# Performance work log

Hardware: AMD Instinct MI355X
Metric: run time of the kernel (lower is better)

The kernel has to match this reference:

```python
import jax, jax.numpy as jnp
import numpy as np
from jax import lax

RATIO = 2.0
ITERATIONS = 1


def setup_inputs() -> dict:
    key = jax.random.key(0)
    k1, k2 = jax.random.split(key)
    N, H, W = 64, 512, 512
    x = jax.random.normal(k1, (N, H, W), dtype=jnp.float32)  # logits
    y = jax.random.randint(k2, (N, H, W), 0, 2, dtype=jnp.int32)  # binary labels
    return {"x": x, "y": y}


def _erode(m):
    # cv2.erode with 3x3 all-ones kernel == 3x3 min-pool; cv2 default border
    # value for erode is +inf, matching reduce_window's init_value padding.
    return lax.reduce_window(m, jnp.inf, lax.min, (1, 3, 3), (1, 1, 1), 'SAME')


def _dilate(m):
    # cv2.dilate == 3x3 max-pool; default border value -inf == init_value pad.
    return lax.reduce_window(m, -jnp.inf, lax.max, (1, 3, 3), (1, 1, 1), 'SAME')


def reference(x, y):
    yf = y.astype(x.dtype)
    # elementwise BCE-with-logits (reduction='none'), numerically stable
    loss = jnp.maximum(x, 0.0) - x * yf + jnp.log1p(jnp.exp(-jnp.abs(x)))
    m = (y > 0).astype(x.dtype)  # [N,H,W] binary mask
    ero, dil = m, m
    for _ in range(ITERATIONS):
        ero = _erode(ero)
        dil = _dilate(dil)
    border = dil - ero  # 1 on border pixels, 0 elsewhere
    w = border * RATIO + (1.0 - border)
    return (loss * w).mean()
```

## Files before the change

### kernel.cpp

```cpp
#include <hip/hip_runtime.h>
#include <math.h>

#define NIMG 64
#define HH 512
#define WW 512
#define TR 8
#define ROWSTRIDE 520
#define LROWS (TR + 2)
#define NBLOCKS (NIMG * (HH / TR))
#define INV_TOTAL (1.0f / 16777216.0f)

__global__ __launch_bounds__(256) void border_loss_main(
    const float* __restrict__ x, const int* __restrict__ y,
    float* __restrict__ part, int atomic_mode)
{
    __shared__ unsigned char flags[LROWS * ROWSTRIDE];
    __shared__ float wsum[4];

    const int tid = threadIdx.x;
    const int nb  = blockIdx.x;
    const int n   = nb >> 6;
    const int R0  = (nb & 63) * TR;
    const long long imgbase = (long long)n * HH * WW;

    if (tid < LROWS) {
        unsigned char* row = &flags[tid * ROWSTRIDE];
        row[0] = 0; row[513] = 0; row[514] = 0; row[515] = 0;
    }

    #pragma unroll
    for (int it = 0; it < 5; ++it) {
        int idx = tid + it * 256;
        int j = idx >> 7;
        int g = idx & 127;
        int gr = R0 - 1 + j;
        unsigned int f4 = 0;
        if ((unsigned)gr < (unsigned)HH) {
            const int4 yv = *(const int4*)(y + imgbase + (long long)gr * WW + 4 * g);
            f4  = (yv.x > 0 ? 1u : 2u);
            f4 |= (yv.y > 0 ? 1u : 2u) << 8;
            f4 |= (yv.z > 0 ? 1u : 2u) << 16;
            f4 |= (yv.w > 0 ? 1u : 2u) << 24;
        }
        unsigned char* p = &flags[j * ROWSTRIDE + 4 * g + 1];
        p[0] = (unsigned char)(f4);
        p[1] = (unsigned char)(f4 >> 8);
        p[2] = (unsigned char)(f4 >> 16);
        p[3] = (unsigned char)(f4 >> 24);
    }
    __syncthreads();

    float acc = 0.0f;

    #pragma unroll
    for (int it = 0; it < 4; ++it) {
        int idx = tid + it * 256;
        int r = idx >> 7;
        int g = idx & 127;
        const unsigned int* l0 = (const unsigned int*)&flags[(r    ) * ROWSTRIDE + 4 * g];
        const unsigned int* l1 = (const unsigned int*)&flags[(r + 1) * ROWSTRIDE + 4 * g];
        const unsigned int* l2 = (const unsigned int*)&flags[(r + 2) * ROWSTRIDE + 4 * g];
        unsigned long long v0 = (unsigned long long)l0[0] | ((unsigned long long)l0[1] << 32);
        unsigned long long v1 = (unsigned long long)l1[0] | ((unsigned long long)l1[1] << 32);
        unsigned long long v2 = (unsigned long long)l2[0] | ((unsigned long long)l2[1] << 32);
        unsigned long long v = v0 | v1 | v2;
        unsigned long long h = v | (v >> 8) | (v >> 16);

        const float4 xv = *(const float4*)(x + imgbase + (long long)(R0 + r) * WW + 4 * g);
        const float xs[4] = {xv.x, xv.y, xv.z, xv.w};
        #pragma unroll
        for (int k = 0; k < 4; ++k) {
            float xf = xs[k];
            float m = (float)((unsigned)(v1 >> (8 * (k + 1))) & 1u);
            float l = fmaxf(xf, 0.0f) - xf * m + log1pf(expf(-fabsf(xf)));
            float wgt = (((unsigned)(h >> (8 * k)) & 3u) == 3u) ? 2.0f : 1.0f;
            acc += l * wgt;
        }
    }

    #pragma unroll
    for (int off = 32; off > 0; off >>= 1)
        acc += __shfl_down(acc, off);
    if ((tid & 63) == 0) wsum[tid >> 6] = acc;
    __syncthreads();
    if (tid == 0) {
        float s = wsum[0] + wsum[1] + wsum[2] + wsum[3];
        if (atomic_mode) atomicAdd(part, s * INV_TOTAL);
        else             part[blockIdx.x] = s;
    }
}

__global__ __launch_bounds__(256) void border_loss_reduce(
    const float* __restrict__ part, float* __restrict__ out)
{
    __shared__ float wsum[4];
    float s = 0.0f;
    for (int i = threadIdx.x; i < NBLOCKS; i += 256) s += part[i];
    #pragma unroll
    for (int off = 32; off > 0; off >>= 1)
        s += __shfl_down(s, off);
    if ((threadIdx.x & 63) == 0) wsum[threadIdx.x >> 6] = s;
    __syncthreads();
    if (threadIdx.x == 0)
        out[0] = (wsum[0] + wsum[1] + wsum[2] + wsum[3]) * INV_TOTAL;
}

__global__ void border_loss_zero(float* out) { out[0] = 0.0f; }

extern "C" void kernel_launch(void* const* d_in, const int* in_sizes, int n_in,
                              void* d_out, int out_size, void* d_ws, size_t ws_size,
                              hipStream_t stream)
{
    const float* x = (const float*)d_in[0];
    const int*   y = (const int*)d_in[1];
    float* out = (float*)d_out;

    if (ws_size >= (size_t)NBLOCKS * sizeof(float)) {
        float* part = (float*)d_ws;
        border_loss_main<<<NBLOCKS, 256, 0, stream>>>(x, y, part, 0);
        border_loss_reduce<<<1, 256, 0, stream>>>(part, out);
    } else {
        border_loss_zero<<<1, 1, 0, stream>>>(out);
        border_loss_main<<<NBLOCKS, 256, 0, stream>>>(x, y, out, 1);
    }
}
```

Before: 169.4 us.

## Encode label masks as wave-ballot bitmasks and compute borders with bit shifts

Replaces the byte-per-pixel shared flag array with 64-bit ballot bitmasks for the mask and its complement. Erosion and dilation become row ORs plus shifts with carries across segments. It also enlarges tiles to 32 rows with 512-thread blocks, which cuts halo rereads of y from 25% to about 6%, and switches to fast __expf/__logf intrinsics. Loads drop from 16-byte vectors to 4-byte per-lane coalesced loads, and the fast math intrinsics may slightly change accuracy.

```diff
diff --git a/kernel.cpp b/kernel.cpp
--- a/kernel.cpp
+++ b/kernel.cpp
@@ -4,87 +4,90 @@
 #define NIMG 64
 #define HH 512
 #define WW 512
-#define TR 8
-#define ROWSTRIDE 520
+#define TR 32
+#define NSEG 8
 #define LROWS (TR + 2)
 #define NBLOCKS (NIMG * (HH / TR))
 #define INV_TOTAL (1.0f / 16777216.0f)
 
-__global__ __launch_bounds__(256) void border_loss_main(
+__global__ __launch_bounds__(512) void border_loss_main(
     const float* __restrict__ x, const int* __restrict__ y,
     float* __restrict__ part, int atomic_mode)
 {
-    __shared__ unsigned char flags[LROWS * ROWSTRIDE];
-    __shared__ float wsum[4];
+    __shared__ unsigned long long mm[LROWS][NSEG];
+    __shared__ unsigned long long mz[LROWS][NSEG];
+    __shared__ float wsum[8];
 
-    const int tid = threadIdx.x;
-    const int nb  = blockIdx.x;
-    const int n   = nb >> 6;
-    const int R0  = (nb & 63) * TR;
+    const int tid  = threadIdx.x;
+    const int lane = tid & 63;
+    const int w    = tid >> 6;
+    const int nb   = blockIdx.x;
+    const int n    = nb >> 4;
+    const int R0   = (nb & 15) * TR;
     const long long imgbase = (long long)n * HH * WW;
 
-    if (tid < LROWS) {
-        unsigned char* row = &flags[tid * ROWSTRIDE];
-        row[0] = 0; row[513] = 0; row[514] = 0; row[515] = 0;
-    }
-
-    #pragma unroll
-    for (int it = 0; it < 5; ++it) {
-        int idx = tid + it * 256;
-        int j = idx >> 7;
-        int g = idx & 127;
+    for (int T = w; T < LROWS * NSEG; T += 8) {
+        int j = T >> 3;
+        int s = T & 7;
         int gr = R0 - 1 + j;
-        unsigned int f4 = 0;
+        unsigned long long bm = 0ull, bz = 0ull;
         if ((unsigned)gr < (unsigned)HH) {
-            const int4 yv = *(const int4*)(y + imgbase + (long long)gr * WW + 4 * g);
-            f4  = (yv.x > 0 ? 1u : 2u);
-            f4 |= (yv.y > 0 ? 1u : 2u) << 8;
-            f4 |= (yv.z > 0 ? 1u : 2u) << 16;
-            f4 |= (yv.w > 0 ? 1u : 2u) << 24;
+            int yv = y[imgbase + (long long)gr * WW + (s << 6) + lane];
+            bm = __ballot(yv > 0);
+            bz = ~bm;
         }
-        unsigned char* p = &flags[j * ROWSTRIDE + 4 * g + 1];
-        p[0] = (unsigned char)(f4);
-        p[1] = (unsigned char)(f4 >> 8);
-        p[2] = (unsigned char)(f4 >> 16);
-        p[3] = (unsigned char)(f4 >> 24);
+        if (lane == 0) { mm[j][s] = bm; mz[j][s] = bz; }
     }
     __syncthreads();
 
     float acc = 0.0f;
+    #pragma unroll
+    for (int k = 0; k < TR / 8; ++k) {
+        int rr = w + (k << 3);
+        int jr = rr + 1;
+        const float* xrow = x + imgbase + (long long)(R0 + rr) * WW;
 
-    #pragma unroll
-    for (int it = 0; it < 4; ++it) {
-        int idx = tid + it * 256;
-        int r = idx >> 7;
-        int g = idx & 127;
-        const unsigned int* l0 = (const unsigned int*)&flags[(r    ) * ROWSTRIDE + 4 * g];
-        const unsigned int* l1 = (const unsigned int*)&flags[(r + 1) * ROWSTRIDE + 4 * g];
-        const unsigned int* l2 = (const unsigned int*)&flags[(r + 2) * ROWSTRIDE + 4 * g];
-        unsigned long long v0 = (unsigned long long)l0[0] | ((unsigned long long)l0[1] << 32);
-        unsigned long long v1 = (unsigned long long)l1[0] | ((unsigned long long)l1[1] << 32);
-        unsigned long long v2 = (unsigned long long)l2[0] | ((unsigned long long)l2[1] << 32);
-        unsigned long long v = v0 | v1 | v2;
-        unsigned long long h = v | (v >> 8) | (v >> 16);
+        unsigned long long vm_prev = 0ull, vz_prev = 0ull;
+        unsigned long long vm_cur = mm[jr-1][0] | mm[jr][0] | mm[jr+1][0];
+        unsigned long long vz_cur = mz[jr-1][0] | mz[jr][0] | mz[jr+1][0];
 
-        const float4 xv = *(const float4*)(x + imgbase + (long long)(R0 + r) * WW + 4 * g);
-        const float xs[4] = {xv.x, xv.y, xv.z, xv.w};
         #pragma unroll
-        for (int k = 0; k < 4; ++k) {
-            float xf = xs[k];
-            float m = (float)((unsigned)(v1 >> (8 * (k + 1))) & 1u);
-            float l = fmaxf(xf, 0.0f) - xf * m + log1pf(expf(-fabsf(xf)));
-            float wgt = (((unsigned)(h >> (8 * k)) & 3u) == 3u) ? 2.0f : 1.0f;
-            acc += l * wgt;
+        for (int s = 0; s < NSEG; ++s) {
+            unsigned long long vm_next = 0ull, vz_next = 0ull;
+            if (s + 1 < NSEG) {
+                vm_next = mm[jr-1][s+1] | mm[jr][s+1] | mm[jr+1][s+1];
+                vz_next = mz[jr-1][s+1] | mz[jr][s+1] | mz[jr+1][s+1];
+            }
+            unsigned long long hm = vm_cur | (vm_cur << 1) | (vm_cur >> 1)
+                                  | (vm_prev >> 63) | (vm_next << 63);
+            unsigned long long hz = vz_cur | (vz_cur << 1) | (vz_cur >> 1)
+                                  | (vz_prev >> 63) | (vz_next << 63);
+            unsigned long long border = hm & hz;
+            unsigned long long mrow   = mm[jr][s];
+
+            float xf = xrow[(s << 6) + lane];
+            float a  = fabsf(xf);
+            float lg = __logf(1.0f + __expf(-a));
+            float mterm = ((mrow >> lane) & 1ull) ? xf : 0.0f;
+            float loss  = fmaxf(xf, 0.0f) - mterm + lg;
+            float wgt   = ((border >> lane) & 1ull) ? 2.0f : 1.0f;
+            acc = fmaf(loss, wgt, acc);
+
+            vm_prev = vm_cur; vz_prev = vz_cur;
+            vm_cur  = vm_next; vz_cur  = vz_next;
         }
     }
 
     #pragma unroll
     for (int off = 32; off > 0; off >>= 1)
         acc += __shfl_down(acc, off);
-    if ((tid & 63) == 0) wsum[tid >> 6] = acc;
+    __syncthreads();
+    if (lane == 0) wsum[w] = acc;
     __syncthreads();
     if (tid == 0) {
-        float s = wsum[0] + wsum[1] + wsum[2] + wsum[3];
+        float s = 0.0f;
+        #pragma unroll
+        for (int i = 0; i < 8; ++i) s += wsum[i];
         if (atomic_mode) atomicAdd(part, s * INV_TOTAL);
         else             part[blockIdx.x] = s;
     }
@@ -117,10 +120,10 @@
 
     if (ws_size >= (size_t)NBLOCKS * sizeof(float)) {
         float* part = (float*)d_ws;
-        border_loss_main<<<NBLOCKS, 256, 0, stream>>>(x, y, part, 0);
+        border_loss_main<<<NBLOCKS, 512, 0, stream>>>(x, y, part, 0);
         border_loss_reduce<<<1, 256, 0, stream>>>(part, out);
     } else {
         border_loss_zero<<<1, 1, 0, stream>>>(out);
-        border_loss_main<<<NBLOCKS, 256, 0, stream>>>(x, y, out, 1);
+        border_loss_main<<<NBLOCKS, 512, 0, stream>>>(x, y, out, 1);
     }
 }
```

After: 164.0 us. -3.2%, faster.

## Replace LDS halo tile with per-wave register row streaming and lane shuffles

Applied to the files above, without the earlier changes.

Each wave now owns a half-row strip of 8 rows and walks down them, keeping the three label rows' flags in registers and exchanging horizontal neighbours with lane shuffles and a scalar boundary load, instead of staging a 10-row halo in shared memory with a block barrier. The next row's x and y are prefetched while the current row is computed. Fast __expf/__logf intrinsics replace log1pf/expf. This removes LDS traffic and the sync, and cuts the halo re-read ratio per tile. In exchange it adds shuffle work and small precision differences from the fast intrinsics.

```diff
diff --git a/kernel.cpp b/kernel.cpp
--- a/kernel.cpp
+++ b/kernel.cpp
@@ -4,89 +4,116 @@
 #define NIMG 64
 #define HH 512
 #define WW 512
-#define TR 8
-#define ROWSTRIDE 520
-#define LROWS (TR + 2)
-#define NBLOCKS (NIMG * (HH / TR))
+#define SH 8
+#define NBLOCKS (NIMG * 32)
 #define INV_TOTAL (1.0f / 16777216.0f)
 
-__global__ __launch_bounds__(256) void border_loss_main(
+typedef unsigned int u32;
+
+__device__ __forceinline__ u32 flags4(int4 yv) {
+    u32 f = (yv.x > 0) ? 1u : 2u;
+    f |= ((yv.y > 0) ? 1u : 2u) << 8;
+    f |= ((yv.z > 0) ? 1u : 2u) << 16;
+    f |= ((yv.w > 0) ? 1u : 2u) << 24;
+    return f;
+}
+
+__global__ __launch_bounds__(256, 8) void border_loss_main(
     const float* __restrict__ x, const int* __restrict__ y,
     float* __restrict__ part, int atomic_mode)
 {
-    __shared__ unsigned char flags[LROWS * ROWSTRIDE];
     __shared__ float wsum[4];
 
-    const int tid = threadIdx.x;
-    const int nb  = blockIdx.x;
-    const int n   = nb >> 6;
-    const int R0  = (nb & 63) * TR;
-    const long long imgbase = (long long)n * HH * WW;
+    const int tid  = threadIdx.x;
+    const int lane = tid & 63;
+    const int w    = tid >> 6;
+    const int b    = blockIdx.x;
+    const int n    = b >> 5;
+    const int q    = ((b & 31) << 2) | w;
+    const int g    = q & 1;
+    const int R0   = (q >> 1) * SH;
+    const int base = n * (HH * WW);
+    const int colv = (g << 8) | (lane << 2);
+    const int cb   = 256 - g;
+    const int*   __restrict__ yb = y + base;
+    const float* __restrict__ xb = x + base;
+    const int idxL = (lane + 63) & 63;
+    const int idxR = (lane + 1) & 63;
 
-    if (tid < LROWS) {
-        unsigned char* row = &flags[tid * ROWSTRIDE];
-        row[0] = 0; row[513] = 0; row[514] = 0; row[515] = 0;
+#define YVEC(row) (*(const int4*)(yb + (row) * WW + colv))
+#define XVEC(row) (*(const float4*)(xb + (row) * WW + colv))
+#define YBND(row) (yb[__builtin_amdgcn_readfirstlane((row) * WW + cb)])
+
+    u32 f_t = 0u, bF_t = 0u;
+    if (R0 > 0) {
+        f_t  = flags4(YVEC(R0 - 1));
+        bF_t = (YBND(R0 - 1) > 0) ? 1u : 2u;
     }
+    u32 f_c  = flags4(YVEC(R0));
+    u32 bF_c = (YBND(R0) > 0) ? 1u : 2u;
+
+    const int pr0 = (R0 + 1 < HH) ? R0 + 1 : HH - 1;
+    int4   y4_b = YVEC(pr0);
+    int    bY_b = YBND(pr0);
+    float4 x4_c = XVEC(R0);
+
+    float acc0 = 0.0f, acc1 = 0.0f;
 
     #pragma unroll
-    for (int it = 0; it < 5; ++it) {
-        int idx = tid + it * 256;
-        int j = idx >> 7;
-        int g = idx & 127;
-        int gr = R0 - 1 + j;
-        unsigned int f4 = 0;
-        if ((unsigned)gr < (unsigned)HH) {
-            const int4 yv = *(const int4*)(y + imgbase + (long long)gr * WW + 4 * g);
-            f4  = (yv.x > 0 ? 1u : 2u);
-            f4 |= (yv.y > 0 ? 1u : 2u) << 8;
-            f4 |= (yv.z > 0 ? 1u : 2u) << 16;
-            f4 |= (yv.w > 0 ? 1u : 2u) << 24;
+    for (int r = 0; r < SH; ++r) {
+        const int gr = R0 + r;
+
+        int4 y4_n; int bY_n; float4 x4_n;
+        if (r < SH - 1) {
+            const int pry = (gr + 2 < HH) ? gr + 2 : HH - 1;
+            y4_n = YVEC(pry);
+            bY_n = YBND(pry);
+            x4_n = XVEC(gr + 1);
         }
-        unsigned char* p = &flags[j * ROWSTRIDE + 4 * g + 1];
-        p[0] = (unsigned char)(f4);
-        p[1] = (unsigned char)(f4 >> 8);
-        p[2] = (unsigned char)(f4 >> 16);
-        p[3] = (unsigned char)(f4 >> 24);
-    }
-    __syncthreads();
 
-    float acc = 0.0f;
+        const bool vB = (gr + 1 < HH);
+        const u32 f_b  = vB ? flags4(y4_b) : 0u;
+        const u32 bF_b = vB ? ((bY_b > 0) ? 1u : 2u) : 0u;
 
-    #pragma unroll
-    for (int it = 0; it < 4; ++it) {
-        int idx = tid + it * 256;
-        int r = idx >> 7;
-        int g = idx & 127;
-        const unsigned int* l0 = (const unsigned int*)&flags[(r    ) * ROWSTRIDE + 4 * g];
-        const unsigned int* l1 = (const unsigned int*)&flags[(r + 1) * ROWSTRIDE + 4 * g];
-        const unsigned int* l2 = (const unsigned int*)&flags[(r + 2) * ROWSTRIDE + 4 * g];
-        unsigned long long v0 = (unsigned long long)l0[0] | ((unsigned long long)l0[1] << 32);
-        unsigned long long v1 = (unsigned long long)l1[0] | ((unsigned long long)l1[1] << 32);
-        unsigned long long v2 = (unsigned long long)l2[0] | ((unsigned long long)l2[1] << 32);
-        unsigned long long v = v0 | v1 | v2;
-        unsigned long long h = v | (v >> 8) | (v >> 16);
+        const u32 v   = f_t | f_c | f_b;
+        const u32 bFv = bF_t | bF_c | bF_b;
+        const u32 vL  = __shfl(v, idxL);
+        const u32 vR  = __shfl(v, idxR);
+        const u32 inL = (lane == 0)  ? (g ? bFv : 0u) : (vL >> 24);
+        const u32 inR = (lane == 63) ? (g ? 0u : bFv) : (vR & 0xffu);
+        const u32 h   = v | (v << 8) | (v >> 8) | inL | (inR << 24);
+        const u32 bm  = h & (h >> 1) & 0x01010101u;
 
-        const float4 xv = *(const float4*)(x + imgbase + (long long)(R0 + r) * WW + 4 * g);
-        const float xs[4] = {xv.x, xv.y, xv.z, xv.w};
+        const float xs[4] = {x4_c.x, x4_c.y, x4_c.z, x4_c.w};
         #pragma unroll
         for (int k = 0; k < 4; ++k) {
-            float xf = xs[k];
-            float m = (float)((unsigned)(v1 >> (8 * (k + 1))) & 1u);
-            float l = fmaxf(xf, 0.0f) - xf * m + log1pf(expf(-fabsf(xf)));
-            float wgt = (((unsigned)(h >> (8 * k)) & 3u) == 3u) ? 2.0f : 1.0f;
-            acc += l * wgt;
+            const float xf = xs[k];
+            const float lg = __logf(1.0f + __expf(-fabsf(xf)));
+            const bool mbit = (f_c >> (8 * k)) & 1u;
+            const bool bbit = (bm  >> (8 * k)) & 1u;
+            const float loss = fmaxf(xf, 0.0f) - (mbit ? xf : 0.0f) + lg;
+            if (k & 1) acc1 = fmaf(loss, bbit ? 2.0f : 1.0f, acc1);
+            else       acc0 = fmaf(loss, bbit ? 2.0f : 1.0f, acc0);
         }
+
+        f_t = f_c;  f_c = f_b;
+        bF_t = bF_c; bF_c = bF_b;
+        if (r < SH - 1) { y4_b = y4_n; bY_b = bY_n; x4_c = x4_n; }
     }
+#undef YVEC
+#undef XVEC
+#undef YBND
 
+    float acc = acc0 + acc1;
     #pragma unroll
     for (int off = 32; off > 0; off >>= 1)
         acc += __shfl_down(acc, off);
-    if ((tid & 63) == 0) wsum[tid >> 6] = acc;
+    if (lane == 0) wsum[w] = acc;
     __syncthreads();
     if (tid == 0) {
-        float s = wsum[0] + wsum[1] + wsum[2] + wsum[3];
-        if (atomic_mode) atomicAdd(part, s * INV_TOTAL);
-        else             part[blockIdx.x] = s;
+        const float t = wsum[0] + wsum[1] + wsum[2] + wsum[3];
+        if (atomic_mode) atomicAdd(part, t * INV_TOTAL);
+        else             part[blockIdx.x] = t;
     }
 }
 
@@ -94,12 +121,12 @@
     const float* __restrict__ part, float* __restrict__ out)
 {
     __shared__ float wsum[4];
-    float s = 0.0f;
-    for (int i = threadIdx.x; i < NBLOCKS; i += 256) s += part[i];
+    float t = 0.0f;
+    for (int i = threadIdx.x; i < NBLOCKS; i += 256) t += part[i];
     #pragma unroll
     for (int off = 32; off > 0; off >>= 1)
-        s += __shfl_down(s, off);
-    if ((threadIdx.x & 63) == 0) wsum[threadIdx.x >> 6] = s;
+        t += __shfl_down(t, off);
+    if ((threadIdx.x & 63) == 0) wsum[threadIdx.x >> 6] = t;
     __syncthreads();
     if (threadIdx.x == 0)
         out[0] = (wsum[0] + wsum[1] + wsum[2] + wsum[3]) * INV_TOTAL;
```

Measured after the change: 188.6 us. 1.11x slower.

## Replace LDS halo tiling with direct global neighbor loads and fast math

Applied to the files above, without the earlier changes.

Removes the shared-memory flag tile and per-block sync; each thread now loads its own float4 of x plus the 3x6 neighbourhood of labels straight from global memory, relying on cache for the redundant row reads. Computes erosion/dilation via bitwise AND/OR on the raw labels. Swaps log1pf/expf for __logf/__expf intrinsics and launches one thread per four pixels with more blocks. Redundant label reads raise cache traffic, and fast intrinsics slightly reduce accuracy.

```diff
diff --git a/kernel.cpp b/kernel.cpp
--- a/kernel.cpp
+++ b/kernel.cpp
@@ -4,78 +4,91 @@
 #define NIMG 64
 #define HH 512
 #define WW 512
-#define TR 8
-#define ROWSTRIDE 520
-#define LROWS (TR + 2)
-#define NBLOCKS (NIMG * (HH / TR))
+#define NPIX (NIMG * HH * WW)
+#define NTHREADS (NPIX / 4)
+#define NBLK (NTHREADS / 256)
 #define INV_TOTAL (1.0f / 16777216.0f)
 
-__global__ __launch_bounds__(256) void border_loss_main(
+__global__ __launch_bounds__(256, 8) void border_loss_main(
     const float* __restrict__ x, const int* __restrict__ y,
     float* __restrict__ part, int atomic_mode)
 {
-    __shared__ unsigned char flags[LROWS * ROWSTRIDE];
     __shared__ float wsum[4];
 
     const int tid = threadIdx.x;
-    const int nb  = blockIdx.x;
-    const int n   = nb >> 6;
-    const int R0  = (nb & 63) * TR;
-    const long long imgbase = (long long)n * HH * WW;
+    const int idx = blockIdx.x * 256 + tid;
+    const int g   = idx & 127;
+    const int r   = (idx >> 7) & (HH - 1);
+    const int n   = idx >> 16;
+    const int rowb = n * (HH * WW) + r * WW;
+    const int c0  = g << 2;
 
-    if (tid < LROWS) {
-        unsigned char* row = &flags[tid * ROWSTRIDE];
-        row[0] = 0; row[513] = 0; row[514] = 0; row[515] = 0;
+    const int offT = (r > 0)      ? -WW : 0;
+    const int offB = (r < HH - 1) ?  WW : 0;
+    const int cL   = (g == 0)     ? 0        : (c0 - 1);
+    const int cR   = (g == 127)   ? (WW - 1) : (c0 + 4);
+
+    const int4 yC = *(const int4*)(y + rowb + c0);
+    const int4 yT = *(const int4*)(y + rowb + offT + c0);
+    const int4 yB = *(const int4*)(y + rowb + offB + c0);
+    const int yCL = y[rowb + cL];
+    const int yTL = y[rowb + offT + cL];
+    const int yBL = y[rowb + offB + cL];
+    const int yCR = y[rowb + cR];
+    const int yTR = y[rowb + offT + cR];
+    const int yBR = y[rowb + offB + cR];
+    const float4 xv = *(const float4*)(x + rowb + c0);
+
+    const int vo0 = yT.x | yC.x | yB.x;
+    const int vo1 = yT.y | yC.y | yB.y;
+    const int vo2 = yT.z | yC.z | yB.z;
+    const int vo3 = yT.w | yC.w | yB.w;
+    const int va0 = yT.x & yC.x & yB.x;
+    const int va1 = yT.y & yC.y & yB.y;
+    const int va2 = yT.z & yC.z & yB.z;
+    const int va3 = yT.w & yC.w & yB.w;
+    const int voL = yTL | yCL | yBL;
+    const int vaL = yTL & yCL & yBL;
+    const int voR = yTR | yCR | yBR;
+    const int vaR = yTR & yCR & yBR;
+
+    const int ho0 = voL | vo0 | vo1;
+    const int ho1 = vo0 | vo1 | vo2;
+    const int ho2 = vo1 | vo2 | vo3;
+    const int ho3 = vo2 | vo3 | voR;
+    const int ha0 = vaL & va0 & va1;
+    const int ha1 = va0 & va1 & va2;
+    const int ha2 = va1 & va2 & va3;
+    const int ha3 = va2 & va3 & vaR;
+
+    float acc;
+    {
+        const float xf = xv.x;
+        const float lg = __logf(1.0f + __expf(-fabsf(xf)));
+        const float ls = fmaxf(xf, 0.0f) - (yC.x ? xf : 0.0f) + lg;
+        const bool bd = (ho0 != 0) & (ha0 == 0);
+        acc = ls * (bd ? 2.0f : 1.0f);
     }
-
-    #pragma unroll
-    for (int it = 0; it < 5; ++it) {
-        int idx = tid + it * 256;
-        int j = idx >> 7;
-        int g = idx & 127;
-        int gr = R0 - 1 + j;
-        unsigned int f4 = 0;
-        if ((unsigned)gr < (unsigned)HH) {
-            const int4 yv = *(const int4*)(y + imgbase + (long long)gr * WW + 4 * g);
-            f4  = (yv.x > 0 ? 1u : 2u);
-            f4 |= (yv.y > 0 ? 1u : 2u) << 8;
-            f4 |= (yv.z > 0 ? 1u : 2u) << 16;
-            f4 |= (yv.w > 0 ? 1u : 2u) << 24;
-        }
-        unsigned char* p = &flags[j * ROWSTRIDE + 4 * g + 1];
-        p[0] = (unsigned char)(f4);
-        p[1] = (unsigned char)(f4 >> 8);
-        p[2] = (unsigned char)(f4 >> 16);
-        p[3] = (unsigned char)(f4 >> 24);
+    {
+        const float xf = xv.y;
+        const float lg = __logf(1.0f + __expf(-fabsf(xf)));
+        const float ls = fmaxf(xf, 0.0f) - (yC.y ? xf : 0.0f) + lg;
+        const bool bd = (ho1 != 0) & (ha1 == 0);
+        acc = fmaf(ls, bd ? 2.0f : 1.0f, acc);
     }
-    __syncthreads();
-
-    float acc = 0.0f;
-
-    #pragma unroll
-    for (int it = 0; it < 4; ++it) {
-        int idx = tid + it * 256;
-        int r = idx >> 7;
-        int g = idx & 127;
-        const unsigned int* l0 = (const unsigned int*)&flags[(r    ) * ROWSTRIDE + 4 * g];
-        const unsigned int* l1 = (const unsigned int*)&flags[(r + 1) * ROWSTRIDE + 4 * g];
-        const unsigned int* l2 = (const unsigned int*)&flags[(r + 2) * ROWSTRIDE + 4 * g];
-        unsigned long long v0 = (unsigned long long)l0[0] | ((unsigned long long)l0[1] << 32);
-        unsigned long long v1 = (unsigned long long)l1[0] | ((unsigned long long)l1[1] << 32);
-        unsigned long long v2 = (unsigned long long)l2[0] | ((unsigned long long)l2[1] << 32);
-        unsigned long long v = v0 | v1 | v2;
-        unsigned long long h = v | (v >> 8) | (v >> 16);
-
-        const float4 xv = *(const float4*)(x + imgbase + (long long)(R0 + r) * WW + 4 * g);
-        const float xs[4] = {xv.x, xv.y, xv.z, xv.w};
-        #pragma unroll
-        for (int k = 0; k < 4; ++k) {
-            float xf = xs[k];
-            float m = (float)((unsigned)(v1 >> (8 * (k + 1))) & 1u);
-            float l = fmaxf(xf, 0.0f) - xf * m + log1pf(expf(-fabsf(xf)));
-            float wgt = (((unsigned)(h >> (8 * k)) & 3u) == 3u) ? 2.0f : 1.0f;
-            acc += l * wgt;
-        }
+    {
+        const float xf = xv.z;
+        const float lg = __logf(1.0f + __expf(-fabsf(xf)));
+        const float ls = fmaxf(xf, 0.0f) - (yC.z ? xf : 0.0f) + lg;
+        const bool bd = (ho2 != 0) & (ha2 == 0);
+        acc = fmaf(ls, bd ? 2.0f : 1.0f, acc);
+    }
+    {
+        const float xf = xv.w;
+        const float lg = __logf(1.0f + __expf(-fabsf(xf)));
+        const float ls = fmaxf(xf, 0.0f) - (yC.w ? xf : 0.0f) + lg;
+        const bool bd = (ho3 != 0) & (ha3 == 0);
+        acc = fmaf(ls, bd ? 2.0f : 1.0f, acc);
     }
 
     #pragma unroll
@@ -84,9 +97,9 @@
     if ((tid & 63) == 0) wsum[tid >> 6] = acc;
     __syncthreads();
     if (tid == 0) {
-        float s = wsum[0] + wsum[1] + wsum[2] + wsum[3];
-        if (atomic_mode) atomicAdd(part, s * INV_TOTAL);
-        else             part[blockIdx.x] = s;
+        const float t = wsum[0] + wsum[1] + wsum[2] + wsum[3];
+        if (atomic_mode) atomicAdd(part, t * INV_TOTAL);
+        else             part[blockIdx.x] = t;
     }
 }
 
@@ -94,12 +107,12 @@
     const float* __restrict__ part, float* __restrict__ out)
 {
     __shared__ float wsum[4];
-    float s = 0.0f;
-    for (int i = threadIdx.x; i < NBLOCKS; i += 256) s += part[i];
+    float t = 0.0f;
+    for (int i = threadIdx.x; i < NBLK; i += 256) t += part[i];
     #pragma unroll
     for (int off = 32; off > 0; off >>= 1)
-        s += __shfl_down(s, off);
-    if ((threadIdx.x & 63) == 0) wsum[threadIdx.x >> 6] = s;
+        t += __shfl_down(t, off);
+    if ((threadIdx.x & 63) == 0) wsum[threadIdx.x >> 6] = t;
     __syncthreads();
     if (threadIdx.x == 0)
         out[0] = (wsum[0] + wsum[1] + wsum[2] + wsum[3]) * INV_TOTAL;
@@ -115,12 +128,12 @@
     const int*   y = (const int*)d_in[1];
     float* out = (float*)d_out;
 
-    if (ws_size >= (size_t)NBLOCKS * sizeof(float)) {
+    if (ws_size >= (size_t)NBLK * sizeof(float)) {
         float* part = (float*)d_ws;
-        border_loss_main<<<NBLOCKS, 256, 0, stream>>>(x, y, part, 0);
+        border_loss_main<<<NBLK, 256, 0, stream>>>(x, y, part, 0);
         border_loss_reduce<<<1, 256, 0, stream>>>(part, out);
     } else {
         border_loss_zero<<<1, 1, 0, stream>>>(out);
-        border_loss_main<<<NBLOCKS, 256, 0, stream>>>(x, y, out, 1);
+        border_loss_main<<<NBLK, 256, 0, stream>>>(x, y, out, 1);
     }
 }
```

New measurement: 159.6 us. -5.8%, faster.
